# Performance work log

Hardware: AMD Instinct MI355X
Metric: run time of the kernel (lower is better)

Reference implementation:

```python
import jax, jax.numpy as jnp
import numpy as np

HID, NH, HD, KTS = 512, 8, 64, 4
BATCH, SEQ = 2, 1024
CLIP, AMIN, AMAX = 2.0, 1e-4, 0.9995
ROPE_BASE = 10000.0


def _rmsnorm(x, w, eps=1e-5):
    rms = jnp.sqrt(jnp.mean(x * x, axis=-1, keepdims=True) + eps)
    return x / rms * w


def _rope(q, k, base=ROPE_BASE):
    # q,k: [B,T,H,D], D even -> rotate-half formulation (split halves, not interleaved)
    T, D = q.shape[1], q.shape[-1]
    half = D // 2
    pos = jnp.arange(T, dtype=q.dtype)
    inv_freq = 1.0 / (base ** (jnp.arange(half, dtype=q.dtype) / half))
    ang = pos[:, None] * inv_freq[None, :]            # [T, half]
    cos = jnp.cos(ang)[None, :, None, :]
    sin = jnp.sin(ang)[None, :, None, :]
    def rot(x):
        x1, x2 = x[..., :half], x[..., half:]
        return jnp.concatenate([x1 * cos - x2 * sin, x1 * sin + x2 * cos], axis=-1)
    return rot(q), rot(k)


def setup_inputs() -> dict:
    key = jax.random.key(0)
    ks = jax.random.split(key, 10)
    def xavier(k, shape):
        lim = float(np.sqrt(6.0 / (shape[0] + shape[1])))
        return jax.random.uniform(k, shape, jnp.float32, -lim, lim)
    x = jax.random.normal(ks[0], (BATCH, SEQ, HID), jnp.float32)
    mask = jnp.ones((BATCH, SEQ), jnp.int32)
    qW = xavier(ks[1], (HID, HID))
    kW = xavier(ks[2], (HID, HID))
    vW = xavier(ks[3], (HID, HID))
    oW = xavier(ks[4], (HID, HID))
    ob = jnp.zeros((HID,), jnp.float32)
    # alpha bias from geometric half-lives [32,128,512,2048]
    half_lives = np.array([32.0 * (4.0 ** i) for i in range(KTS)], dtype=np.float64)
    alphas = np.clip(np.exp(-np.log(2.0) / half_lives), AMIN, AMAX)
    alphas = np.tile(alphas, NH)
    ab = jnp.asarray(np.log(alphas / (1.0 - alphas)), jnp.float32)
    aW = 0.01 * jax.random.normal(ks[5], (NH * KTS, HID), jnp.float32)
    mW = 0.01 * jax.random.normal(ks[6], (NH * KTS, HID), jnp.float32)
    mb = jnp.zeros((NH * KTS,), jnp.float32)
    in_w = jnp.ones((HID,), jnp.float32)
    kn_w = jnp.ones((HD,), jnp.float32)
    vn_w = jnp.ones((HD,), jnp.float32)
    ln_w = jnp.ones((HID,), jnp.float32)
    ln_b = jnp.zeros((HID,), jnp.float32)
    return dict(x=x, in_w=in_w, qW=qW, kW=kW, vW=vW, aW=aW, ab=ab, mW=mW, mb=mb,
                oW=oW, ob=ob, kn_w=kn_w, vn_w=vn_w, ln_w=ln_w, ln_b=ln_b, mask=mask)


def reference(x, in_w, qW, kW, vW, aW, ab, mW, mb, oW, ob, kn_w, vn_w, ln_w, ln_b, mask):
    B, T, _ = x.shape
    xn = _rmsnorm(x, in_w)
    q = (xn @ qW.T).reshape(B, T, NH, HD)
    k = (xn @ kW.T).reshape(B, T, NH, HD)
    v = (xn @ vW.T).reshape(B, T, NH, HD)
    q, k = _rope(q, k)
    k = _rmsnorm(k, kn_w)
    v = _rmsnorm(v, vn_w)
    alpha = jnp.clip(jax.nn.sigmoid(xn @ aW.T + ab), AMIN, AMAX).reshape(B, T, NH, KTS)
    mix = jax.nn.softmax((xn @ mW.T + mb).reshape(B, T, NH, KTS), axis=-1)
    m = mask.astype(jnp.float32)
    c = float(np.sqrt(HD)) * CLIP

    def step(h, inp):
        # h: [B,H,K,D,D] fp32 state; delta-rule write + multi-timescale decay + norm clip
        q_t, k_t, v_t, a_t, mx_t, m_t = inp
        outer = (k_t * m_t[:, None, None])[:, :, None, :, None] * v_t[:, :, None, None, :]
        h = h * a_t[..., None, None] + outer
        norm = jnp.sqrt(jnp.sum(h * h, axis=(-2, -1), keepdims=True))
        h = h * jnp.minimum(c / (norm + 1e-6), 1.0)
        y = jnp.einsum('bhd,bhkde->bhke', q_t, h)
        return h, jnp.einsum('bhk,bhkd->bhd', mx_t, y)

    h0 = jnp.zeros((B, NH, KTS, HD, HD), jnp.float32)
    tm = lambda a: jnp.moveaxis(a, 1, 0)  # time-major
    xs = (tm(q), tm(k), tm(v), tm(alpha), tm(mix), m.T)
    _, ys = jax.lax.scan(jax.checkpoint(step), h0, xs)  # ys: [T,B,H,D]
    y = jnp.moveaxis(ys, 0, 1).reshape(B, T, HID)
    out = y @ oW.T + ob  # dropout p=0 (eval)
    r = x + out
    mu = jnp.mean(r, axis=-1, keepdims=True)
    var = jnp.mean((r - mu) ** 2, axis=-1, keepdims=True)
    return (r - mu) / jnp.sqrt(var + 1e-5) * ln_w + ln_b
```

## Files before the change

### kernel.cpp

```cpp
#include <hip/hip_runtime.h>
#include <math.h>

#define SEQT 1024
#define NTOK 2048
#define HIDN 512
#define NHD 8
#define HDIM 64
#define KTSN 4

__device__ __forceinline__ float wred(float v) {
#pragma unroll
  for (int off = 32; off; off >>= 1) v += __shfl_xor(v, off, 64);
  return v;
}

template <int CTRL>
__device__ __forceinline__ float rra(float v) {
  return v + __int_as_float(__builtin_amdgcn_update_dpp(
                 0, __float_as_int(v), CTRL, 0xf, 0xf, true));
}
__device__ __forceinline__ float rlane(float v, int l) {
  return __int_as_float(__builtin_amdgcn_readlane(__float_as_int(v), l));
}
__device__ __forceinline__ float wsum64_fast(float v) {
  v = rra<0x121>(v);
  v = rra<0x122>(v);
  v = rra<0x124>(v);
  v = rra<0x128>(v);
  return (rlane(v, 0) + rlane(v, 16)) + (rlane(v, 32) + rlane(v, 48));
}

__global__ __launch_bounds__(256) void k_rmsnorm_in(
    const float* __restrict__ x, const float* __restrict__ w, float* __restrict__ xn) {
  int m = blockIdx.x;
  int tid = threadIdx.x;
  const float* row = x + (size_t)m * HIDN;
  float2 v = *(const float2*)(row + tid * 2);
  float ss = wred(v.x * v.x + v.y * v.y);
  __shared__ float red[4];
  int lane = tid & 63, wv = tid >> 6;
  if (lane == 0) red[wv] = ss;
  __syncthreads();
  float tot = red[0] + red[1] + red[2] + red[3];
  float inv = rsqrtf(tot * (1.0f / HIDN) + 1e-5f);
  float2 wv2 = *(const float2*)(w + tid * 2);
  float2 o;
  o.x = v.x * inv * wv2.x;
  o.y = v.y * inv * wv2.y;
  *(float2*)(xn + (size_t)m * HIDN + tid * 2) = o;
}

__global__ __launch_bounds__(256) void k_gemm_qkv(
    const float* __restrict__ A, const float* __restrict__ Bq,
    const float* __restrict__ Bk, const float* __restrict__ Bv,
    float* __restrict__ Cq, float* __restrict__ Ck, float* __restrict__ Cv) {
  __shared__ __align__(16) float As[32][68];
  __shared__ __align__(16) float Bs0[32][68];
  __shared__ __align__(16) float Bs1[32][68];
  __shared__ __align__(16) float Bs2[32][68];
  int tid = threadIdx.x;
  int m0 = blockIdx.x * 64, n0 = blockIdx.y * 64;
  int tm = tid >> 4, tn = tid & 15;
  float aq[4][4] = {}, ak[4][4] = {}, av4[4][4] = {};
  int rr = tid >> 2, cc = (tid & 3) * 8;
  for (int k0 = 0; k0 < HIDN; k0 += 32) {
    const float* s0 = A + (size_t)(m0 + rr) * HIDN + k0 + cc;
    float4 a0 = *(const float4*)s0;
    float4 a1 = *(const float4*)(s0 + 4);
    As[cc + 0][rr] = a0.x; As[cc + 1][rr] = a0.y; As[cc + 2][rr] = a0.z; As[cc + 3][rr] = a0.w;
    As[cc + 4][rr] = a1.x; As[cc + 5][rr] = a1.y; As[cc + 6][rr] = a1.z; As[cc + 7][rr] = a1.w;
    size_t boff = (size_t)(n0 + rr) * HIDN + k0 + cc;
    float4 b0 = *(const float4*)(Bq + boff);
    float4 b1 = *(const float4*)(Bq + boff + 4);
    Bs0[cc + 0][rr] = b0.x; Bs0[cc + 1][rr] = b0.y; Bs0[cc + 2][rr] = b0.z; Bs0[cc + 3][rr] = b0.w;
    Bs0[cc + 4][rr] = b1.x; Bs0[cc + 5][rr] = b1.y; Bs0[cc + 6][rr] = b1.z; Bs0[cc + 7][rr] = b1.w;
    b0 = *(const float4*)(Bk + boff);
    b1 = *(const float4*)(Bk + boff + 4);
    Bs1[cc + 0][rr] = b0.x; Bs1[cc + 1][rr] = b0.y; Bs1[cc + 2][rr] = b0.z; Bs1[cc + 3][rr] = b0.w;
    Bs1[cc + 4][rr] = b1.x; Bs1[cc + 5][rr] = b1.y; Bs1[cc + 6][rr] = b1.z; Bs1[cc + 7][rr] = b1.w;
    b0 = *(const float4*)(Bv + boff);
    b1 = *(const float4*)(Bv + boff + 4);
    Bs2[cc + 0][rr] = b0.x; Bs2[cc + 1][rr] = b0.y; Bs2[cc + 2][rr] = b0.z; Bs2[cc + 3][rr] = b0.w;
    Bs2[cc + 4][rr] = b1.x; Bs2[cc + 5][rr] = b1.y; Bs2[cc + 6][rr] = b1.z; Bs2[cc + 7][rr] = b1.w;
    __syncthreads();
#pragma unroll
    for (int kk = 0; kk < 32; ++kk) {
      float4 a4 = *(const float4*)&As[kk][tm * 4];
      float4 q4 = *(const float4*)&Bs0[kk][tn * 4];
      float4 k4 = *(const float4*)&Bs1[kk][tn * 4];
      float4 v4 = *(const float4*)&Bs2[kk][tn * 4];
      float aa[4] = {a4.x, a4.y, a4.z, a4.w};
      float qq[4] = {q4.x, q4.y, q4.z, q4.w};
      float kk_[4] = {k4.x, k4.y, k4.z, k4.w};
      float vv[4] = {v4.x, v4.y, v4.z, v4.w};
#pragma unroll
      for (int i = 0; i < 4; ++i)
#pragma unroll
        for (int j = 0; j < 4; ++j) {
          aq[i][j] = fmaf(aa[i], qq[j], aq[i][j]);
          ak[i][j] = fmaf(aa[i], kk_[j], ak[i][j]);
          av4[i][j] = fmaf(aa[i], vv[j], av4[i][j]);
        }
    }
    __syncthreads();
  }
#pragma unroll
  for (int i = 0; i < 4; ++i) {
    size_t mr = (size_t)(m0 + tm * 4 + i) * HIDN;
#pragma unroll
    for (int j = 0; j < 4; ++j) {
      int nc = n0 + tn * 4 + j;
      Cq[mr + nc] = aq[i][j];
      Ck[mr + nc] = ak[i][j];
      Cv[mr + nc] = av4[i][j];
    }
  }
}

__global__ __launch_bounds__(256) void k_gemm_am(
    const float* __restrict__ A, const float* __restrict__ Ba,
    const float* __restrict__ Bm, float* __restrict__ Ca, float* __restrict__ Cm) {
  __shared__ __align__(16) float As[32][68];
  __shared__ __align__(16) float Bs[32][68];
  int tid = threadIdx.x;
  int m0 = blockIdx.x * 64;
  int tm = tid >> 4, tn = tid & 15;
  float acc[4][4] = {};
  int rr = tid >> 2, cc = (tid & 3) * 8;
  for (int k0 = 0; k0 < HIDN; k0 += 32) {
    const float* s0 = A + (size_t)(m0 + rr) * HIDN + k0 + cc;
    float4 a0 = *(const float4*)s0;
    float4 a1 = *(const float4*)(s0 + 4);
    As[cc + 0][rr] = a0.x; As[cc + 1][rr] = a0.y; As[cc + 2][rr] = a0.z; As[cc + 3][rr] = a0.w;
    As[cc + 4][rr] = a1.x; As[cc + 5][rr] = a1.y; As[cc + 6][rr] = a1.z; As[cc + 7][rr] = a1.w;
    const float* s1 = ((rr < 32) ? (Ba + (size_t)rr * HIDN) : (Bm + (size_t)(rr - 32) * HIDN)) + k0 + cc;
    float4 b0 = *(const float4*)s1;
    float4 b1 = *(const float4*)(s1 + 4);
    Bs[cc + 0][rr] = b0.x; Bs[cc + 1][rr] = b0.y; Bs[cc + 2][rr] = b0.z; Bs[cc + 3][rr] = b0.w;
    Bs[cc + 4][rr] = b1.x; Bs[cc + 5][rr] = b1.y; Bs[cc + 6][rr] = b1.z; Bs[cc + 7][rr] = b1.w;
    __syncthreads();
#pragma unroll
    for (int kk = 0; kk < 32; ++kk) {
      float4 a4 = *(const float4*)&As[kk][tm * 4];
      float4 b4 = *(const float4*)&Bs[kk][tn * 4];
      float aa[4] = {a4.x, a4.y, a4.z, a4.w};
      float bb[4] = {b4.x, b4.y, b4.z, b4.w};
#pragma unroll
      for (int i = 0; i < 4; ++i)
#pragma unroll
        for (int j = 0; j < 4; ++j) acc[i][j] = fmaf(aa[i], bb[j], acc[i][j]);
    }
    __syncthreads();
  }
#pragma unroll
  for (int i = 0; i < 4; ++i) {
    int mr = m0 + tm * 4 + i;
#pragma unroll
    for (int j = 0; j < 4; ++j) {
      int nc = tn * 4 + j;
      if (nc < 32)
        Ca[(size_t)mr * 32 + nc] = acc[i][j];
      else
        Cm[(size_t)mr * 32 + nc - 32] = acc[i][j];
    }
  }
}

__global__ __launch_bounds__(256) void k_rope_table(float2* __restrict__ tab) {
  int idx = blockIdx.x * 256 + threadIdx.x;
  int t = idx >> 5, j = idx & 31;
  float invf = (float)exp2(-(double)j * (13.287712379549449 / 32.0));
  float ang = (float)t * invf;
  double s, c;
  sincos((double)ang, &s, &c);
  tab[idx] = make_float2((float)c, (float)s);
}

__global__ __launch_bounds__(256) void k_postproc(
    const float* __restrict__ q_in, const float* __restrict__ k_in, const float* __restrict__ v_in,
    const float* __restrict__ a_pre, const float* __restrict__ m_pre,
    const float* __restrict__ ab, const float* __restrict__ mb,
    const float* __restrict__ kn_w, const float* __restrict__ vn_w,
    const float2* __restrict__ tab,
    float* __restrict__ qh, float* __restrict__ kh, float* __restrict__ vh,
    float* __restrict__ av, float* __restrict__ mv,
    float* __restrict__ qkd, float* __restrict__ kvq) {
  int wid = blockIdx.x * 4 + (threadIdx.x >> 6);
  int lane = threadIdx.x & 63;
  int b = wid >> 13;
  int rem = wid & 8191;
  int t = rem >> 3;
  int h = rem & 7;
  size_t src = (size_t)(b * SEQT + t) * HIDN + h * HDIM + lane;
  float qv = q_in[src], kv = k_in[src], vv = v_in[src];
  float2 cs = tab[t * 32 + (lane & 31)];
  float qpart = __shfl_xor(qv, 32, 64);
  float kpart = __shfl_xor(kv, 32, 64);
  float qr = (lane < 32) ? (qv * cs.x - qpart * cs.y) : (qpart * cs.y + qv * cs.x);
  float kr = (lane < 32) ? (kv * cs.x - kpart * cs.y) : (kpart * cs.y + kv * cs.x);
  float kss = wred(kr * kr);
  float kn = kr * rsqrtf(kss * (1.0f / HDIM) + 1e-5f) * kn_w[lane];
  float vss = wred(vv * vv);
  float vn = vv * rsqrtf(vss * (1.0f / HDIM) + 1e-5f) * vn_w[lane];
  size_t dst = ((size_t)(b * NHD + h) * SEQT + t) * HDIM + lane;
  qh[dst] = qr;
  kh[dst] = kn;
  vh[dst] = vn;
  float knss = wred(kn * kn);
  float vnss = wred(vn * vn);
  float qkdot = wred(qr * kn);
  if (lane == 0) {
    size_t sdst = (size_t)(b * NHD + h) * SEQT + t;
    qkd[sdst] = qkdot;
    kvq[sdst] = knss * vnss;
  }
  if (lane < 4) {
    int col = h * 4 + lane;
    float pa = a_pre[(size_t)(b * SEQT + t) * 32 + col] + ab[col];
    float al = 1.0f / (1.0f + expf(-pa));
    al = fminf(fmaxf(al, 1e-4f), 0.9995f);
    float pm = m_pre[(size_t)(b * SEQT + t) * 32 + col] + mb[col];
    float mx = pm;
    mx = fmaxf(mx, __shfl_xor(mx, 1, 64));
    mx = fmaxf(mx, __shfl_xor(mx, 2, 64));
    float e = expf(pm - mx);
    float sum = e;
    sum += __shfl_xor(sum, 1, 64);
    sum += __shfl_xor(sum, 2, 64);
    size_t adst = ((size_t)(b * NHD + h) * KTSN + lane) * SEQT + t;
    av[adst] = al;
    mv[adst] = e / sum;
  }
}

__global__ __launch_bounds__(256) void k_cross(
    const float* __restrict__ qh, const float* __restrict__ kh, const float* __restrict__ vh,
    float* __restrict__ kkx, float* __restrict__ vvx, float* __restrict__ qxx) {
  int wid = blockIdx.x * 4 + (threadIdx.x >> 6);
  int lane = threadIdx.x & 63;
  int bh = wid >> 10;
  int t = wid & 1023;
  size_t sidx = (size_t)bh * SEQT + t;
  if (t == 0) {
    if (lane == 0) { kkx[sidx] = 0.f; vvx[sidx] = 0.f; qxx[sidx] = 0.f; }
    return;
  }
  size_t base = (size_t)bh * SEQT * HDIM;
  float kc = kh[base + (size_t)t * HDIM + lane];
  float kp = kh[base + (size_t)(t - 1) * HDIM + lane];
  float vc = vh[base + (size_t)t * HDIM + lane];
  float vpv = vh[base + (size_t)(t - 1) * HDIM + lane];
  float qc = qh[base + (size_t)t * HDIM + lane];
  float s1 = wred(kc * kp);
  float s2 = wred(vc * vpv);
  float s3 = wred(qc * kp);
  if (lane == 0) { kkx[sidx] = s1; vvx[sidx] = s2; qxx[sidx] = s3; }
}

#define G16P(X) \
  X(0, 0) X(1, 1) X(2, 2) X(3, 3) X(4, 0) X(5, 1) X(6, 2) X(7, 3) \
  X(8, 0) X(9, 1) X(10, 2) X(11, 3) X(12, 0) X(13, 1) X(14, 2) X(15, 3)

#define DECLH(g, a) float h##g = 0.f;
#define HUP0(g, a) h##g = fmaf(h##g, ag0, rlane(kqj0, (g)) * vm0);
#define HUP1(g, a) h##g = fmaf(h##g, ag1, rlane(kqj1, (g)) * vm1);
#define MV4(g, a)                                   \
  {                                                 \
    float k2_ = rlane(kqj2, (g));                   \
    float q2_ = rlane(kqj2, 16 + (g));              \
    float k3_ = rlane(kqj3, (g));                   \
    float q3_ = rlane(kqj3, 16 + (g));              \
    zk2##a = fmaf(k2_, h##g, zk2##a);               \
    zk3##a = fmaf(k3_, h##g, zk3##a);               \
    pv2##a = fmaf(q2_, h##g, pv2##a);               \
    pv3##a = fmaf(q3_, h##g, pv3##a);               \
  }

__global__ __launch_bounds__(256, 1) void k_scan(
    const float* __restrict__ qh, const float* __restrict__ kh, const float* __restrict__ vh,
    const float* __restrict__ av, const float* __restrict__ mv, const int* __restrict__ mask,
    const float* __restrict__ qkd, const float* __restrict__ kvq,
    const float* __restrict__ kkx, const float* __restrict__ vvx, const float* __restrict__ qxx,
    float* __restrict__ y0p, float* __restrict__ y1p, float* __restrict__ y2p,
    float* __restrict__ y3p) {
  int c = blockIdx.x;
  int kt = c & 3;
  int bh = c >> 2;
  int b = bh >> 3;
  int h = bh & 7;
  int tid = threadIdx.x;
  int w = tid >> 6;
  int lane = tid & 63;
  int dbase = w * 16;

  const float* kp = kh + (size_t)bh * SEQT * HDIM;
  const float* qp = qh + (size_t)bh * SEQT * HDIM;
  const float* vp = vh + (size_t)bh * SEQT * HDIM;
  const float* ap = av + (size_t)c * SEQT;
  const float* mp = mv + (size_t)c * SEQT;
  const float* qkp = qkd + (size_t)bh * SEQT;
  const float* kvp = kvq + (size_t)bh * SEQT;
  const float* kkp = kkx + (size_t)bh * SEQT;
  const float* vvp = vvx + (size_t)bh * SEQT;
  const float* qxp = qxx + (size_t)bh * SEQT;
  const int* mk = mask + (size_t)b * SEQT;
  float* ysel = (kt == 0) ? y0p : (kt == 1) ? y1p : (kt == 2) ? y2p : y3p;
  float* ypo = ysel + (size_t)(b * SEQT) * HIDN + h * HDIM + lane;

  __shared__ __align__(16) float2 Zb[2][4];
  __shared__ __align__(16) float Pb[2][2][4][64];
  __shared__ int cnt;

  G16P(DECLH)
  float gprev = 1.0f;
  float usq = 0.0f;

  int off = lane & 15;
  const float* kqbase = ((lane >> 4) & 1) ? qp : kp;
  int kqidx = dbase + off;

  float kqj0 = kqbase[kqidx];
  float kqj1 = kqbase[(size_t)1 * HDIM + kqidx];
  float kqj2 = kqbase[(size_t)2 * HDIM + kqidx];
  float kqj3 = kqbase[(size_t)3 * HDIM + kqidx];
  float kqj4 = kqbase[(size_t)4 * HDIM + kqidx];
  float kqj5 = kqbase[(size_t)5 * HDIM + kqidx];
  float vj0 = vp[lane], vj1 = vp[HDIM + lane], vj2 = vp[2 * HDIM + lane];
  float vj3 = vp[3 * HDIM + lane], vj4 = vp[4 * HDIM + lane], vj5 = vp[5 * HDIM + lane];
  float a0 = ap[0], a1 = ap[1], a2 = ap[2], a3 = ap[3], a4 = ap[4], a5 = ap[5];
  float mx0 = mp[0], mx1 = mp[1], mx2 = mp[2], mx3 = mp[3], mx4 = mp[4], mx5 = mp[5];
  float m0 = (float)mk[0], m1 = (float)mk[1], m2 = (float)mk[2];
  float m3 = (float)mk[3], m4 = (float)mk[4], m5 = (float)mk[5];
  float qk0 = qkp[0], qk1 = qkp[1], qk2 = qkp[2], qk3 = qkp[3], qk4 = qkp[4], qk5 = qkp[5];
  float kv0 = kvp[0], kv1 = kvp[1], kv2 = kvp[2], kv3 = kvp[3], kv4 = kvp[4], kv5 = kvp[5];
  float kko0 = kkp[1], kko1 = kkp[3], kko2 = kkp[5];
  float vvo0 = vvp[1], vvo1 = vvp[3], vvo2 = vvp[5];
  float qxo0 = qxp[1], qxo1 = qxp[3], qxo2 = qxp[5];

  if (tid == 0) cnt = 0;
  if (lane == 0) Zb[0][w] = make_float2(0.f, 0.f);
  Pb[0][0][w][lane] = 0.f;
  Pb[0][1][w][lane] = 0.f;
  __syncthreads();

  for (int s = 0; s < SEQT; s += 2) {
    int r = s >> 1;
    int P = r & 1;
    int t6 = s + 6, t7 = s + 7;
    if (t6 > SEQT - 1) t6 = SEQT - 1;
    if (t7 > SEQT - 1) t7 = SEQT - 1;
    float kqN6 = kqbase[(size_t)t6 * HDIM + kqidx];
    float kqN7 = kqbase[(size_t)t7 * HDIM + kqidx];
    float vN6 = vp[(size_t)t6 * HDIM + lane];
    float vN7 = vp[(size_t)t7 * HDIM + lane];
    float aN6 = ap[t6], aN7 = ap[t7];
    float mxN6 = mp[t6], mxN7 = mp[t7];
    float mN6 = (float)mk[t6], mN7 = (float)mk[t7];
    float qkN6 = qkp[t6], qkN7 = qkp[t7];
    float kvN6 = kvp[t6], kvN7 = kvp[t7];
    float kkN = kkp[t7], vvN = vvp[t7], qxN = qxp[t7];

    float2 zb0 = Zb[P][0], zb1 = Zb[P][1], zb2 = Zb[P][2], zb3 = Zb[P][3];
    float zs = (zb0.x + zb1.x) + (zb2.x + zb3.x);
    float w1 = (zb0.y + zb1.y) + (zb2.y + zb3.y);

    float ag0 = a0 * gprev;
    float vm0 = m0 * vj0;
    G16P(HUP0)
    float usq0 = fmaf(ag0 * ag0, usq, fmaf(2.0f * ag0 * m0, zs, (m0 * m0) * kv0));
    usq0 = fmaxf(usq0, 0.0f);
    float g0 = fminf(16.0f * rsqrtf(usq0), 1.0f);

    float z1 = fmaf(ag0, w1, (m0 * kko0) * vvo0);
    float ag1 = a1 * g0;
    float vm1 = m1 * vj1;
    G16P(HUP1)
    float usq1 = fmaf(ag1 * ag1, usq0, fmaf(2.0f * ag1 * m1, z1, (m1 * m1) * kv1));
    usq1 = fmaxf(usq1, 0.0f);
    float g1 = fminf(16.0f * rsqrtf(usq1), 1.0f);

    float zk20 = 0.f, zk21 = 0.f, zk22 = 0.f, zk23 = 0.f;
    float zk30 = 0.f, zk31 = 0.f, zk32 = 0.f, zk33 = 0.f;
    float pv20 = 0.f, pv21 = 0.f, pv22 = 0.f, pv23 = 0.f;
    float pv30 = 0.f, pv31 = 0.f, pv32 = 0.f, pv33 = 0.f;
    G16P(MV4)
    float zk2s = (zk20 + zk21) + (zk22 + zk23);
    float zk3s = (zk30 + zk31) + (zk32 + zk33);
    float Z0n = wsum64_fast(zk2s * vj2);
    float Z1n = wsum64_fast(zk3s * vj3);
    float P0n = (pv20 + pv21) + (pv22 + pv23);
    float P1n = (pv30 + pv31) + (pv32 + pv33);

    if (w == 0) {
      float pe = (Pb[P][0][0][lane] + Pb[P][0][1][lane]) +
                 (Pb[P][0][2][lane] + Pb[P][0][3][lane]);
      ypo[(size_t)s * HIDN] = (g0 * mx0) * fmaf(ag0, pe, (m0 * qk0) * vj0);
    } else if (w == 1) {
      float pe = (Pb[P][1][0][lane] + Pb[P][1][1][lane]) +
                 (Pb[P][1][2][lane] + Pb[P][1][3][lane]);
      float p1 = fmaf(ag0, pe, (m0 * qxo0) * vj0);
      ypo[(size_t)(s + 1) * HIDN] = (g1 * mx1) * fmaf(ag1, p1, (m1 * qk1) * vj1);
    }

    if (lane == 0) Zb[P ^ 1][w] = make_float2(Z0n, Z1n);
    Pb[P ^ 1][0][w][lane] = P0n;
    Pb[P ^ 1][1][w][lane] = P1n;
    asm volatile("s_waitcnt lgkmcnt(0)" ::: "memory");
    if (lane == 0) atomicAdd(&cnt, 1);
    {
      int target = 4 * (r + 1);
      while (*(volatile int*)&cnt < target) {
      }
    }
    asm volatile("" ::: "memory");

    gprev = g1;
    usq = usq1;
    kqj0 = kqj2; kqj1 = kqj3; kqj2 = kqj4; kqj3 = kqj5; kqj4 = kqN6; kqj5 = kqN7;
    vj0 = vj2; vj1 = vj3; vj2 = vj4; vj3 = vj5; vj4 = vN6; vj5 = vN7;
    a0 = a2; a1 = a3; a2 = a4; a3 = a5; a4 = aN6; a5 = aN7;
    mx0 = mx2; mx1 = mx3; mx2 = mx4; mx3 = mx5; mx4 = mxN6; mx5 = mxN7;
    m0 = m2; m1 = m3; m2 = m4; m3 = m5; m4 = mN6; m5 = mN7;
    qk0 = qk2; qk1 = qk3; qk2 = qk4; qk3 = qk5; qk4 = qkN6; qk5 = qkN7;
    kv0 = kv2; kv1 = kv3; kv2 = kv4; kv3 = kv5; kv4 = kvN6; kv5 = kvN7;
    kko0 = kko1; kko1 = kko2; kko2 = kkN;
    vvo0 = vvo1; vvo1 = vvo2; vvo2 = vvN;
    qxo0 = qxo1; qxo1 = qxo2; qxo2 = qxN;
  }
}

__global__ __launch_bounds__(256) void k_gemm_out(
    const float* __restrict__ y0, const float* __restrict__ y1,
    const float* __restrict__ y2, const float* __restrict__ y3,
    const float* __restrict__ oW, const float* __restrict__ ob,
    const float* __restrict__ x, float* __restrict__ r) {
  __shared__ __align__(16) float As[32][68];
  __shared__ __align__(16) float Bs[32][68];
  int tid = threadIdx.x;
  int m0 = blockIdx.x * 64, n0 = blockIdx.y * 64;
  int tm = tid >> 4, tn = tid & 15;
  float acc[4][4] = {};
  int rr = tid >> 2, cc = (tid & 3) * 8;
  for (int k0 = 0; k0 < HIDN; k0 += 32) {
    size_t aoff = (size_t)(m0 + rr) * HIDN + k0 + cc;
#pragma unroll
    for (int half = 0; half < 2; ++half) {
      size_t sh = aoff + half * 4;
      float4 p0 = *(const float4*)(y0 + sh);
      float4 p1 = *(const float4*)(y1 + sh);
      float4 p2 = *(const float4*)(y2 + sh);
      float4 p3 = *(const float4*)(y3 + sh);
      int cbase = cc + half * 4;
      As[cbase + 0][rr] = p0.x + p1.x + p2.x + p3.x;
      As[cbase + 1][rr] = p0.y + p1.y + p2.y + p3.y;
      As[cbase + 2][rr] = p0.z + p1.z + p2.z + p3.z;
      As[cbase + 3][rr] = p0.w + p1.w + p2.w + p3.w;
    }
    const float* s1 = oW + (size_t)(n0 + rr) * HIDN + k0 + cc;
    float4 b0 = *(const float4*)s1;
    float4 b1 = *(const float4*)(s1 + 4);
    Bs[cc + 0][rr] = b0.x; Bs[cc + 1][rr] = b0.y; Bs[cc + 2][rr] = b0.z; Bs[cc + 3][rr] = b0.w;
    Bs[cc + 4][rr] = b1.x; Bs[cc + 5][rr] = b1.y; Bs[cc + 6][rr] = b1.z; Bs[cc + 7][rr] = b1.w;
    __syncthreads();
#pragma unroll
    for (int kk = 0; kk < 32; ++kk) {
      float4 a4 = *(const float4*)&As[kk][tm * 4];
      float4 b4 = *(const float4*)&Bs[kk][tn * 4];
      float aa[4] = {a4.x, a4.y, a4.z, a4.w};
      float bb[4] = {b4.x, b4.y, b4.z, b4.w};
#pragma unroll
      for (int i = 0; i < 4; ++i)
#pragma unroll
        for (int j = 0; j < 4; ++j) acc[i][j] += aa[i] * bb[j];
    }
    __syncthreads();
  }
#pragma unroll
  for (int i = 0; i < 4; ++i) {
    int mr = m0 + tm * 4 + i;
#pragma unroll
    for (int j = 0; j < 4; ++j) {
      int nc = n0 + tn * 4 + j;
      r[(size_t)mr * HIDN + nc] = x[(size_t)mr * HIDN + nc] + acc[i][j] + ob[nc];
    }
  }
}

__global__ __launch_bounds__(256) void k_layernorm(
    const float* __restrict__ r, const float* __restrict__ w, const float* __restrict__ bb,
    float* __restrict__ out) {
  int m = blockIdx.x;
  int tid = threadIdx.x;
  const float* row = r + (size_t)m * HIDN;
  float2 v = *(const float2*)(row + tid * 2);
  float s = wred(v.x + v.y);
  float ss = wred(v.x * v.x + v.y * v.y);
  __shared__ float r1[4], r2[4];
  int lane = tid & 63, wv = tid >> 6;
  if (lane == 0) {
    r1[wv] = s;
    r2[wv] = ss;
  }
  __syncthreads();
  float S = r1[0] + r1[1] + r1[2] + r1[3];
  float SS = r2[0] + r2[1] + r2[2] + r2[3];
  float mu = S * (1.0f / HIDN);
  float var = SS * (1.0f / HIDN) - mu * mu;
  float inv = rsqrtf(var + 1e-5f);
  float2 w2 = *(const float2*)(w + tid * 2);
  float2 b2 = *(const float2*)(bb + tid * 2);
  float2 o;
  o.x = (v.x - mu) * inv * w2.x + b2.x;
  o.y = (v.y - mu) * inv * w2.y + b2.y;
  *(float2*)(out + (size_t)m * HIDN + tid * 2) = o;
}

extern "C" void kernel_launch(void* const* d_in, const int* in_sizes, int n_in,
                              void* d_out, int out_size, void* d_ws, size_t ws_size,
                              hipStream_t stream) {
  const float* x = (const float*)d_in[0];
  const float* in_w = (const float*)d_in[1];
  const float* qW = (const float*)d_in[2];
  const float* kW = (const float*)d_in[3];
  const float* vW = (const float*)d_in[4];
  const float* aW = (const float*)d_in[5];
  const float* ab = (const float*)d_in[6];
  const float* mW = (const float*)d_in[7];
  const float* mb = (const float*)d_in[8];
  const float* oW = (const float*)d_in[9];
  const float* ob = (const float*)d_in[10];
  const float* kn_w = (const float*)d_in[11];
  const float* vn_w = (const float*)d_in[12];
  const float* ln_w = (const float*)d_in[13];
  const float* ln_b = (const float*)d_in[14];
  const int* mask = (const int*)d_in[15];

  float* ws = (float*)d_ws;
  float* xn = ws + 0;
  float* qb = ws + 1048576;
  float* kb = ws + 2097152;
  float* vb = ws + 3145728;
  float* apre = ws + 4194304;
  float* mpre = ws + 4259840;
  float2* tab = (float2*)(ws + 4325376);
  float* qh = ws + 4390912;
  float* kh = ws + 5439488;
  float* vh = ws + 6488064;
  float* avv = ws + 7536640;
  float* mvv = ws + 7602176;
  float* y3 = ws + 7667712;
  float* y0 = qb;
  float* y1 = kb;
  float* y2 = vb;
  float* rr = xn;
  float* qkd = ws + 0;
  float* kvq = ws + 16384;
  float* kkx = ws + 32768;
  float* vvx = ws + 49152;
  float* qxx = ws + 65536;

  k_rope_table<<<128, 256, 0, stream>>>(tab);
  k_rmsnorm_in<<<NTOK, 256, 0, stream>>>(x, in_w, xn);
  dim3 gBig(32, 8);
  k_gemm_qkv<<<gBig, 256, 0, stream>>>(xn, qW, kW, vW, qb, kb, vb);
  k_gemm_am<<<32, 256, 0, stream>>>(xn, aW, mW, apre, mpre);
  k_postproc<<<4096, 256, 0, stream>>>(qb, kb, vb, apre, mpre, ab, mb, kn_w, vn_w, tab,
                                       qh, kh, vh, avv, mvv, qkd, kvq);
  k_cross<<<4096, 256, 0, stream>>>(qh, kh, vh, kkx, vvx, qxx);
  k_scan<<<64, 256, 0, stream>>>(qh, kh, vh, avv, mvv, mask, qkd, kvq, kkx, vvx, qxx,
                                 y0, y1, y2, y3);
  k_gemm_out<<<gBig, 256, 0, stream>>>(y0, y1, y2, y3, oW, ob, x, rr);
  k_layernorm<<<NTOK, 256, 0, stream>>>(rr, ln_w, ln_b, (float*)d_out);
  (void)in_sizes; (void)n_in; (void)out_size; (void)ws_size;
}
```

Baseline: 702.0 us.

## Split scan state rows across eight waves instead of four

```diff
diff --git a/kernel.cpp b/kernel.cpp
--- a/kernel.cpp
+++ b/kernel.cpp
@@ -257,9 +257,8 @@
   if (lane == 0) { kkx[sidx] = s1; vvx[sidx] = s2; qxx[sidx] = s3; }
 }
 
-#define G16P(X) \
-  X(0, 0) X(1, 1) X(2, 2) X(3, 3) X(4, 0) X(5, 1) X(6, 2) X(7, 3) \
-  X(8, 0) X(9, 1) X(10, 2) X(11, 3) X(12, 0) X(13, 1) X(14, 2) X(15, 3)
+#define G8P(X) \
+  X(0, 0) X(1, 1) X(2, 2) X(3, 3) X(4, 0) X(5, 1) X(6, 2) X(7, 3)
 
 #define DECLH(g, a) float h##g = 0.f;
 #define HUP0(g, a) h##g = fmaf(h##g, ag0, rlane(kqj0, (g)) * vm0);
@@ -267,16 +266,16 @@
 #define MV4(g, a)                                   \
   {                                                 \
     float k2_ = rlane(kqj2, (g));                   \
-    float q2_ = rlane(kqj2, 16 + (g));              \
+    float q2_ = rlane(kqj2, 8 + (g));               \
     float k3_ = rlane(kqj3, (g));                   \
-    float q3_ = rlane(kqj3, 16 + (g));              \
+    float q3_ = rlane(kqj3, 8 + (g));               \
     zk2##a = fmaf(k2_, h##g, zk2##a);               \
     zk3##a = fmaf(k3_, h##g, zk3##a);               \
     pv2##a = fmaf(q2_, h##g, pv2##a);               \
     pv3##a = fmaf(q3_, h##g, pv3##a);               \
   }
 
-__global__ __launch_bounds__(256, 1) void k_scan(
+__global__ __launch_bounds__(512, 1) void k_scan(
     const float* __restrict__ qh, const float* __restrict__ kh, const float* __restrict__ vh,
     const float* __restrict__ av, const float* __restrict__ mv, const int* __restrict__ mask,
     const float* __restrict__ qkd, const float* __restrict__ kvq,
@@ -291,7 +290,7 @@
   int tid = threadIdx.x;
   int w = tid >> 6;
   int lane = tid & 63;
-  int dbase = w * 16;
+  int dbase = w * 8;
 
   const float* kp = kh + (size_t)bh * SEQT * HDIM;
   const float* qp = qh + (size_t)bh * SEQT * HDIM;
@@ -307,16 +306,17 @@
   float* ysel = (kt == 0) ? y0p : (kt == 1) ? y1p : (kt == 2) ? y2p : y3p;
   float* ypo = ysel + (size_t)(b * SEQT) * HIDN + h * HDIM + lane;
 
-  __shared__ __align__(16) float2 Zb[2][4];
-  __shared__ __align__(16) float Pb[2][2][4][64];
+  __shared__ __align__(16) float Z0b[2][8];
+  __shared__ __align__(16) float Z1b[2][8];
+  __shared__ __align__(16) float Pb[2][2][8][64];
   __shared__ int cnt;
 
-  G16P(DECLH)
+  G8P(DECLH)
   float gprev = 1.0f;
   float usq = 0.0f;
 
-  int off = lane & 15;
-  const float* kqbase = ((lane >> 4) & 1) ? qp : kp;
+  int off = lane & 7;
+  const float* kqbase = ((lane >> 3) & 1) ? qp : kp;
   int kqidx = dbase + off;
 
   float kqj0 = kqbase[kqidx];
@@ -338,7 +338,7 @@
   float qxo0 = qxp[1], qxo1 = qxp[3], qxo2 = qxp[5];
 
   if (tid == 0) cnt = 0;
-  if (lane == 0) Zb[0][w] = make_float2(0.f, 0.f);
+  if (lane == 0) { Z0b[0][w] = 0.f; Z1b[0][w] = 0.f; }
   Pb[0][0][w][lane] = 0.f;
   Pb[0][1][w][lane] = 0.f;
   __syncthreads();
@@ -360,13 +360,16 @@
     float kvN6 = kvp[t6], kvN7 = kvp[t7];
     float kkN = kkp[t7], vvN = vvp[t7], qxN = qxp[t7];
 
-    float2 zb0 = Zb[P][0], zb1 = Zb[P][1], zb2 = Zb[P][2], zb3 = Zb[P][3];
-    float zs = (zb0.x + zb1.x) + (zb2.x + zb3.x);
-    float w1 = (zb0.y + zb1.y) + (zb2.y + zb3.y);
+    float4 za = *(const float4*)&Z0b[P][0];
+    float4 zb = *(const float4*)&Z0b[P][4];
+    float zs = ((za.x + za.y) + (za.z + za.w)) + ((zb.x + zb.y) + (zb.z + zb.w));
+    float4 wa = *(const float4*)&Z1b[P][0];
+    float4 wb = *(const float4*)&Z1b[P][4];
+    float w1 = ((wa.x + wa.y) + (wa.z + wa.w)) + ((wb.x + wb.y) + (wb.z + wb.w));
 
     float ag0 = a0 * gprev;
     float vm0 = m0 * vj0;
-    G16P(HUP0)
+    G8P(HUP0)
     float usq0 = fmaf(ag0 * ag0, usq, fmaf(2.0f * ag0 * m0, zs, (m0 * m0) * kv0));
     usq0 = fmaxf(usq0, 0.0f);
     float g0 = fminf(16.0f * rsqrtf(usq0), 1.0f);
@@ -374,7 +377,7 @@
     float z1 = fmaf(ag0, w1, (m0 * kko0) * vvo0);
     float ag1 = a1 * g0;
     float vm1 = m1 * vj1;
-    G16P(HUP1)
+    G8P(HUP1)
     float usq1 = fmaf(ag1 * ag1, usq0, fmaf(2.0f * ag1 * m1, z1, (m1 * m1) * kv1));
     usq1 = fmaxf(usq1, 0.0f);
     float g1 = fminf(16.0f * rsqrtf(usq1), 1.0f);
@@ -383,7 +386,7 @@
     float zk30 = 0.f, zk31 = 0.f, zk32 = 0.f, zk33 = 0.f;
     float pv20 = 0.f, pv21 = 0.f, pv22 = 0.f, pv23 = 0.f;
     float pv30 = 0.f, pv31 = 0.f, pv32 = 0.f, pv33 = 0.f;
-    G16P(MV4)
+    G8P(MV4)
     float zk2s = (zk20 + zk21) + (zk22 + zk23);
     float zk3s = (zk30 + zk31) + (zk32 + zk33);
     float Z0n = wsum64_fast(zk2s * vj2);
@@ -392,23 +395,27 @@
     float P1n = (pv30 + pv31) + (pv32 + pv33);
 
     if (w == 0) {
-      float pe = (Pb[P][0][0][lane] + Pb[P][0][1][lane]) +
-                 (Pb[P][0][2][lane] + Pb[P][0][3][lane]);
+      float pe = ((Pb[P][0][0][lane] + Pb[P][0][1][lane]) +
+                  (Pb[P][0][2][lane] + Pb[P][0][3][lane])) +
+                 ((Pb[P][0][4][lane] + Pb[P][0][5][lane]) +
+                  (Pb[P][0][6][lane] + Pb[P][0][7][lane]));
       ypo[(size_t)s * HIDN] = (g0 * mx0) * fmaf(ag0, pe, (m0 * qk0) * vj0);
     } else if (w == 1) {
-      float pe = (Pb[P][1][0][lane] + Pb[P][1][1][lane]) +
-                 (Pb[P][1][2][lane] + Pb[P][1][3][lane]);
+      float pe = ((Pb[P][1][0][lane] + Pb[P][1][1][lane]) +
+                  (Pb[P][1][2][lane] + Pb[P][1][3][lane])) +
+                 ((Pb[P][1][4][lane] + Pb[P][1][5][lane]) +
+                  (Pb[P][1][6][lane] + Pb[P][1][7][lane]));
       float p1 = fmaf(ag0, pe, (m0 * qxo0) * vj0);
       ypo[(size_t)(s + 1) * HIDN] = (g1 * mx1) * fmaf(ag1, p1, (m1 * qk1) * vj1);
     }
 
-    if (lane == 0) Zb[P ^ 1][w] = make_float2(Z0n, Z1n);
+    if (lane == 0) { Z0b[P ^ 1][w] = Z0n; Z1b[P ^ 1][w] = Z1n; }
     Pb[P ^ 1][0][w][lane] = P0n;
     Pb[P ^ 1][1][w][lane] = P1n;
     asm volatile("s_waitcnt lgkmcnt(0)" ::: "memory");
     if (lane == 0) atomicAdd(&cnt, 1);
     {
-      int target = 4 * (r + 1);
+      int target = 8 * (r + 1);
       while (*(volatile int*)&cnt < target) {
       }
     }
@@ -567,7 +574,7 @@
   k_postproc<<<4096, 256, 0, stream>>>(qb, kb, vb, apre, mpre, ab, mb, kn_w, vn_w, tab,
                                        qh, kh, vh, avv, mvv, qkd, kvq);
   k_cross<<<4096, 256, 0, stream>>>(qh, kh, vh, kkx, vvx, qxx);
-  k_scan<<<64, 256, 0, stream>>>(qh, kh, vh, avv, mvv, mask, qkd, kvq, kkx, vvx, qxx,
+  k_scan<<<64, 512, 0, stream>>>(qh, kh, vh, avv, mvv, mask, qkd, kvq, kkx, vvx, qxx,
                                  y0, y1, y2, y3);
   k_gemm_out<<<gBig, 256, 0, stream>>>(y0, y1, y2, y3, oW, ob, x, rr);
   k_layernorm<<<NTOK, 256, 0, stream>>>(rr, ln_w, ln_b, (float*)d_out);
```

Measured after the change: 753.7 us. 1.07x slower.

## Interleave two timescale chains per scan block to hide barrier latency

Applied to the files above, without the earlier changes.

```diff
diff --git a/kernel.cpp b/kernel.cpp
--- a/kernel.cpp
+++ b/kernel.cpp
@@ -261,19 +261,32 @@
   X(0, 0) X(1, 1) X(2, 2) X(3, 3) X(4, 0) X(5, 1) X(6, 2) X(7, 3) \
   X(8, 0) X(9, 1) X(10, 2) X(11, 3) X(12, 0) X(13, 1) X(14, 2) X(15, 3)
 
-#define DECLH(g, a) float h##g = 0.f;
-#define HUP0(g, a) h##g = fmaf(h##g, ag0, rlane(kqj0, (g)) * vm0);
-#define HUP1(g, a) h##g = fmaf(h##g, ag1, rlane(kqj1, (g)) * vm1);
-#define MV4(g, a)                                   \
+#define DECLH(g, a) float hA##g = 0.f, hB##g = 0.f;
+#define HUP0A(g, a) hA##g = fmaf(hA##g, ag0, rlane(kqj0, (g)) * vm0);
+#define HUP1A(g, a) hA##g = fmaf(hA##g, ag1, rlane(kqj1, (g)) * vm1);
+#define HUP0B(g, a) hB##g = fmaf(hB##g, ag0, rlane(kqj0, (g)) * vm0);
+#define HUP1B(g, a) hB##g = fmaf(hB##g, ag1, rlane(kqj1, (g)) * vm1);
+#define MV4A(g, a)                                  \
   {                                                 \
     float k2_ = rlane(kqj2, (g));                   \
     float q2_ = rlane(kqj2, 16 + (g));              \
     float k3_ = rlane(kqj3, (g));                   \
     float q3_ = rlane(kqj3, 16 + (g));              \
-    zk2##a = fmaf(k2_, h##g, zk2##a);               \
-    zk3##a = fmaf(k3_, h##g, zk3##a);               \
-    pv2##a = fmaf(q2_, h##g, pv2##a);               \
-    pv3##a = fmaf(q3_, h##g, pv3##a);               \
+    zk2##a = fmaf(k2_, hA##g, zk2##a);              \
+    zk3##a = fmaf(k3_, hA##g, zk3##a);              \
+    pv2##a = fmaf(q2_, hA##g, pv2##a);              \
+    pv3##a = fmaf(q3_, hA##g, pv3##a);              \
+  }
+#define MV4B(g, a)                                  \
+  {                                                 \
+    float k2_ = rlane(kqj2, (g));                   \
+    float q2_ = rlane(kqj2, 16 + (g));              \
+    float k3_ = rlane(kqj3, (g));                   \
+    float q3_ = rlane(kqj3, 16 + (g));              \
+    zk2##a = fmaf(k2_, hB##g, zk2##a);              \
+    zk3##a = fmaf(k3_, hB##g, zk3##a);              \
+    pv2##a = fmaf(q2_, hB##g, pv2##a);              \
+    pv3##a = fmaf(q3_, hB##g, pv3##a);              \
   }
 
 __global__ __launch_bounds__(256, 1) void k_scan(
@@ -283,9 +296,9 @@
     const float* __restrict__ kkx, const float* __restrict__ vvx, const float* __restrict__ qxx,
     float* __restrict__ y0p, float* __restrict__ y1p, float* __restrict__ y2p,
     float* __restrict__ y3p) {
-  int c = blockIdx.x;
-  int kt = c & 3;
-  int bh = c >> 2;
+  int bhp = blockIdx.x;
+  int bh = bhp >> 1;
+  int pair = bhp & 1;
   int b = bh >> 3;
   int h = bh & 7;
   int tid = threadIdx.x;
@@ -296,24 +309,30 @@
   const float* kp = kh + (size_t)bh * SEQT * HDIM;
   const float* qp = qh + (size_t)bh * SEQT * HDIM;
   const float* vp = vh + (size_t)bh * SEQT * HDIM;
-  const float* ap = av + (size_t)c * SEQT;
-  const float* mp = mv + (size_t)c * SEQT;
+  const float* apA = av + (size_t)(bh * 4 + 2 * pair + 0) * SEQT;
+  const float* apB = av + (size_t)(bh * 4 + 2 * pair + 1) * SEQT;
+  const float* mpA = mv + (size_t)(bh * 4 + 2 * pair + 0) * SEQT;
+  const float* mpB = mv + (size_t)(bh * 4 + 2 * pair + 1) * SEQT;
   const float* qkp = qkd + (size_t)bh * SEQT;
   const float* kvp = kvq + (size_t)bh * SEQT;
   const float* kkp = kkx + (size_t)bh * SEQT;
   const float* vvp = vvx + (size_t)bh * SEQT;
   const float* qxp = qxx + (size_t)bh * SEQT;
   const int* mk = mask + (size_t)b * SEQT;
-  float* ysel = (kt == 0) ? y0p : (kt == 1) ? y1p : (kt == 2) ? y2p : y3p;
-  float* ypo = ysel + (size_t)(b * SEQT) * HIDN + h * HDIM + lane;
-
-  __shared__ __align__(16) float2 Zb[2][4];
-  __shared__ __align__(16) float Pb[2][2][4][64];
-  __shared__ int cnt;
+  float* yselA = (pair == 0) ? y0p : y2p;
+  float* yselB = (pair == 0) ? y1p : y3p;
+  float* ypoA = yselA + (size_t)(b * SEQT) * HIDN + h * HDIM + lane;
+  float* ypoB = yselB + (size_t)(b * SEQT) * HIDN + h * HDIM + lane;
+
+  __shared__ __align__(16) float2 ZA[2][4];
+  __shared__ __align__(16) float2 ZB[2][4];
+  __shared__ __align__(16) float PbA[2][2][4][64];
+  __shared__ __align__(16) float PbB[2][2][4][64];
+  __shared__ int cntA, cntB;
 
   G16P(DECLH)
-  float gprev = 1.0f;
-  float usq = 0.0f;
+  float gprevA = 1.0f, usqA = 0.0f;
+  float gprevB = 1.0f, usqB = 0.0f;
 
   int off = lane & 15;
   const float* kqbase = ((lane >> 4) & 1) ? qp : kp;
@@ -327,8 +346,6 @@
   float kqj5 = kqbase[(size_t)5 * HDIM + kqidx];
   float vj0 = vp[lane], vj1 = vp[HDIM + lane], vj2 = vp[2 * HDIM + lane];
   float vj3 = vp[3 * HDIM + lane], vj4 = vp[4 * HDIM + lane], vj5 = vp[5 * HDIM + lane];
-  float a0 = ap[0], a1 = ap[1], a2 = ap[2], a3 = ap[3], a4 = ap[4], a5 = ap[5];
-  float mx0 = mp[0], mx1 = mp[1], mx2 = mp[2], mx3 = mp[3], mx4 = mp[4], mx5 = mp[5];
   float m0 = (float)mk[0], m1 = (float)mk[1], m2 = (float)mk[2];
   float m3 = (float)mk[3], m4 = (float)mk[4], m5 = (float)mk[5];
   float qk0 = qkp[0], qk1 = qkp[1], qk2 = qkp[2], qk3 = qkp[3], qk4 = qkp[4], qk5 = qkp[5];
@@ -336,11 +353,15 @@
   float kko0 = kkp[1], kko1 = kkp[3], kko2 = kkp[5];
   float vvo0 = vvp[1], vvo1 = vvp[3], vvo2 = vvp[5];
   float qxo0 = qxp[1], qxo1 = qxp[3], qxo2 = qxp[5];
-
-  if (tid == 0) cnt = 0;
-  if (lane == 0) Zb[0][w] = make_float2(0.f, 0.f);
-  Pb[0][0][w][lane] = 0.f;
-  Pb[0][1][w][lane] = 0.f;
+  float aA0 = apA[0], aA1 = apA[1], aA2 = apA[2], aA3 = apA[3], aA4 = apA[4], aA5 = apA[5];
+  float aB0 = apB[0], aB1 = apB[1], aB2 = apB[2], aB3 = apB[3], aB4 = apB[4], aB5 = apB[5];
+  float mxA0 = mpA[0], mxA1 = mpA[1], mxA2 = mpA[2], mxA3 = mpA[3], mxA4 = mpA[4], mxA5 = mpA[5];
+  float mxB0 = mpB[0], mxB1 = mpB[1], mxB2 = mpB[2], mxB3 = mpB[3], mxB4 = mpB[4], mxB5 = mpB[5];
+
+  if (tid == 0) { cntA = 0; cntB = 0; }
+  if (lane == 0) { ZA[0][w] = make_float2(0.f, 0.f); ZB[0][w] = make_float2(0.f, 0.f); }
+  PbA[0][0][w][lane] = 0.f; PbA[0][1][w][lane] = 0.f;
+  PbB[0][0][w][lane] = 0.f; PbB[0][1][w][lane] = 0.f;
   __syncthreads();
 
   for (int s = 0; s < SEQT; s += 2) {
@@ -353,79 +374,136 @@
     float kqN7 = kqbase[(size_t)t7 * HDIM + kqidx];
     float vN6 = vp[(size_t)t6 * HDIM + lane];
     float vN7 = vp[(size_t)t7 * HDIM + lane];
-    float aN6 = ap[t6], aN7 = ap[t7];
-    float mxN6 = mp[t6], mxN7 = mp[t7];
     float mN6 = (float)mk[t6], mN7 = (float)mk[t7];
     float qkN6 = qkp[t6], qkN7 = qkp[t7];
     float kvN6 = kvp[t6], kvN7 = kvp[t7];
     float kkN = kkp[t7], vvN = vvp[t7], qxN = qxp[t7];
-
-    float2 zb0 = Zb[P][0], zb1 = Zb[P][1], zb2 = Zb[P][2], zb3 = Zb[P][3];
-    float zs = (zb0.x + zb1.x) + (zb2.x + zb3.x);
-    float w1 = (zb0.y + zb1.y) + (zb2.y + zb3.y);
-
-    float ag0 = a0 * gprev;
+    float aAN6 = apA[t6], aAN7 = apA[t7], aBN6 = apB[t6], aBN7 = apB[t7];
+    float mxAN6 = mpA[t6], mxAN7 = mpA[t7], mxBN6 = mpB[t6], mxBN7 = mpB[t7];
+
     float vm0 = m0 * vj0;
-    G16P(HUP0)
-    float usq0 = fmaf(ag0 * ag0, usq, fmaf(2.0f * ag0 * m0, zs, (m0 * m0) * kv0));
-    usq0 = fmaxf(usq0, 0.0f);
-    float g0 = fminf(16.0f * rsqrtf(usq0), 1.0f);
-
-    float z1 = fmaf(ag0, w1, (m0 * kko0) * vvo0);
-    float ag1 = a1 * g0;
     float vm1 = m1 * vj1;
-    G16P(HUP1)
-    float usq1 = fmaf(ag1 * ag1, usq0, fmaf(2.0f * ag1 * m1, z1, (m1 * m1) * kv1));
-    usq1 = fmaxf(usq1, 0.0f);
-    float g1 = fminf(16.0f * rsqrtf(usq1), 1.0f);
-
-    float zk20 = 0.f, zk21 = 0.f, zk22 = 0.f, zk23 = 0.f;
-    float zk30 = 0.f, zk31 = 0.f, zk32 = 0.f, zk33 = 0.f;
-    float pv20 = 0.f, pv21 = 0.f, pv22 = 0.f, pv23 = 0.f;
-    float pv30 = 0.f, pv31 = 0.f, pv32 = 0.f, pv33 = 0.f;
-    G16P(MV4)
-    float zk2s = (zk20 + zk21) + (zk22 + zk23);
-    float zk3s = (zk30 + zk31) + (zk32 + zk33);
-    float Z0n = wsum64_fast(zk2s * vj2);
-    float Z1n = wsum64_fast(zk3s * vj3);
-    float P0n = (pv20 + pv21) + (pv22 + pv23);
-    float P1n = (pv30 + pv31) + (pv32 + pv33);
-
-    if (w == 0) {
-      float pe = (Pb[P][0][0][lane] + Pb[P][0][1][lane]) +
-                 (Pb[P][0][2][lane] + Pb[P][0][3][lane]);
-      ypo[(size_t)s * HIDN] = (g0 * mx0) * fmaf(ag0, pe, (m0 * qk0) * vj0);
-    } else if (w == 1) {
-      float pe = (Pb[P][1][0][lane] + Pb[P][1][1][lane]) +
-                 (Pb[P][1][2][lane] + Pb[P][1][3][lane]);
-      float p1 = fmaf(ag0, pe, (m0 * qxo0) * vj0);
-      ypo[(size_t)(s + 1) * HIDN] = (g1 * mx1) * fmaf(ag1, p1, (m1 * qk1) * vj1);
-    }
-
-    if (lane == 0) Zb[P ^ 1][w] = make_float2(Z0n, Z1n);
-    Pb[P ^ 1][0][w][lane] = P0n;
-    Pb[P ^ 1][1][w][lane] = P1n;
-    asm volatile("s_waitcnt lgkmcnt(0)" ::: "memory");
-    if (lane == 0) atomicAdd(&cnt, 1);
+
     {
-      int target = 4 * (r + 1);
-      while (*(volatile int*)&cnt < target) {
+      int target = 4 * r;
+      while (*(volatile int*)&cntA < target) {
       }
     }
     asm volatile("" ::: "memory");
-
-    gprev = g1;
-    usq = usq1;
+    {
+      float2 zb0 = ZA[P][0], zb1 = ZA[P][1], zb2 = ZA[P][2], zb3 = ZA[P][3];
+      float zs = (zb0.x + zb1.x) + (zb2.x + zb3.x);
+      float w1 = (zb0.y + zb1.y) + (zb2.y + zb3.y);
+
+      float ag0 = aA0 * gprevA;
+      G16P(HUP0A)
+      float usq0 = fmaf(ag0 * ag0, usqA, fmaf(2.0f * ag0 * m0, zs, (m0 * m0) * kv0));
+      usq0 = fmaxf(usq0, 0.0f);
+      float g0 = fminf(16.0f * rsqrtf(usq0), 1.0f);
+
+      float z1 = fmaf(ag0, w1, (m0 * kko0) * vvo0);
+      float ag1 = aA1 * g0;
+      G16P(HUP1A)
+      float usq1 = fmaf(ag1 * ag1, usq0, fmaf(2.0f * ag1 * m1, z1, (m1 * m1) * kv1));
+      usq1 = fmaxf(usq1, 0.0f);
+      float g1 = fminf(16.0f * rsqrtf(usq1), 1.0f);
+
+      float zk20 = 0.f, zk21 = 0.f, zk22 = 0.f, zk23 = 0.f;
+      float zk30 = 0.f, zk31 = 0.f, zk32 = 0.f, zk33 = 0.f;
+      float pv20 = 0.f, pv21 = 0.f, pv22 = 0.f, pv23 = 0.f;
+      float pv30 = 0.f, pv31 = 0.f, pv32 = 0.f, pv33 = 0.f;
+      G16P(MV4A)
+      float Z0n = wsum64_fast(((zk20 + zk21) + (zk22 + zk23)) * vj2);
+      float Z1n = wsum64_fast(((zk30 + zk31) + (zk32 + zk33)) * vj3);
+      float P0n = (pv20 + pv21) + (pv22 + pv23);
+      float P1n = (pv30 + pv31) + (pv32 + pv33);
+
+      if (w == 0) {
+        float pe = (PbA[P][0][0][lane] + PbA[P][0][1][lane]) +
+                   (PbA[P][0][2][lane] + PbA[P][0][3][lane]);
+        ypoA[(size_t)s * HIDN] = (g0 * mxA0) * fmaf(ag0, pe, (m0 * qk0) * vj0);
+      } else if (w == 1) {
+        float pe = (PbA[P][1][0][lane] + PbA[P][1][1][lane]) +
+                   (PbA[P][1][2][lane] + PbA[P][1][3][lane]);
+        float p1 = fmaf(ag0, pe, (m0 * qxo0) * vj0);
+        ypoA[(size_t)(s + 1) * HIDN] = (g1 * mxA1) * fmaf(ag1, p1, (m1 * qk1) * vj1);
+      }
+
+      if (lane == 0) ZA[P ^ 1][w] = make_float2(Z0n, Z1n);
+      PbA[P ^ 1][0][w][lane] = P0n;
+      PbA[P ^ 1][1][w][lane] = P1n;
+      asm volatile("s_waitcnt lgkmcnt(0)" ::: "memory");
+      if (lane == 0) atomicAdd(&cntA, 1);
+      gprevA = g1;
+      usqA = usq1;
+    }
+
+    {
+      int target = 4 * r;
+      while (*(volatile int*)&cntB < target) {
+      }
+    }
+    asm volatile("" ::: "memory");
+    {
+      float2 zb0 = ZB[P][0], zb1 = ZB[P][1], zb2 = ZB[P][2], zb3 = ZB[P][3];
+      float zs = (zb0.x + zb1.x) + (zb2.x + zb3.x);
+      float w1 = (zb0.y + zb1.y) + (zb2.y + zb3.y);
+
+      float ag0 = aB0 * gprevB;
+      G16P(HUP0B)
+      float usq0 = fmaf(ag0 * ag0, usqB, fmaf(2.0f * ag0 * m0, zs, (m0 * m0) * kv0));
+      usq0 = fmaxf(usq0, 0.0f);
+      float g0 = fminf(16.0f * rsqrtf(usq0), 1.0f);
+
+      float z1 = fmaf(ag0, w1, (m0 * kko0) * vvo0);
+      float ag1 = aB1 * g0;
+      G16P(HUP1B)
+      float usq1 = fmaf(ag1 * ag1, usq0, fmaf(2.0f * ag1 * m1, z1, (m1 * m1) * kv1));
+      usq1 = fmaxf(usq1, 0.0f);
+      float g1 = fminf(16.0f * rsqrtf(usq1), 1.0f);
+
+      float zk20 = 0.f, zk21 = 0.f, zk22 = 0.f, zk23 = 0.f;
+      float zk30 = 0.f, zk31 = 0.f, zk32 = 0.f, zk33 = 0.f;
+      float pv20 = 0.f, pv21 = 0.f, pv22 = 0.f, pv23 = 0.f;
+      float pv30 = 0.f, pv31 = 0.f, pv32 = 0.f, pv33 = 0.f;
+      G16P(MV4B)
+      float Z0n = wsum64_fast(((zk20 + zk21) + (zk22 + zk23)) * vj2);
+      float Z1n = wsum64_fast(((zk30 + zk31) + (zk32 + zk33)) * vj3);
+      float P0n = (pv20 + pv21) + (pv22 + pv23);
+      float P1n = (pv30 + pv31) + (pv32 + pv33);
+
+      if (w == 2) {
+        float pe = (PbB[P][0][0][lane] + PbB[P][0][1][lane]) +
+                   (PbB[P][0][2][lane] + PbB[P][0][3][lane]);
+        ypoB[(size_t)s * HIDN] = (g0 * mxB0) * fmaf(ag0, pe, (m0 * qk0) * vj0);
+      } else if (w == 3) {
+        float pe = (PbB[P][1][0][lane] + PbB[P][1][1][lane]) +
+                   (PbB[P][1][2][lane] + PbB[P][1][3][lane]);
+        float p1 = fmaf(ag0, pe, (m0 * qxo0) * vj0);
+        ypoB[(size_t)(s + 1) * HIDN] = (g1 * mxB1) * fmaf(ag1, p1, (m1 * qk1) * vj1);
+      }
+
+      if (lane == 0) ZB[P ^ 1][w] = make_float2(Z0n, Z1n);
+      PbB[P ^ 1][0][w][lane] = P0n;
+      PbB[P ^ 1][1][w][lane] = P1n;
+      asm volatile("s_waitcnt lgkmcnt(0)" ::: "memory");
+      if (lane == 0) atomicAdd(&cntB, 1);
+      gprevB = g1;
+      usqB = usq1;
+    }
+
     kqj0 = kqj2; kqj1 = kqj3; kqj2 = kqj4; kqj3 = kqj5; kqj4 = kqN6; kqj5 = kqN7;
     vj0 = vj2; vj1 = vj3; vj2 = vj4; vj3 = vj5; vj4 = vN6; vj5 = vN7;
-    a0 = a2; a1 = a3; a2 = a4; a3 = a5; a4 = aN6; a5 = aN7;
-    mx0 = mx2; mx1 = mx3; mx2 = mx4; mx3 = mx5; mx4 = mxN6; mx5 = mxN7;
     m0 = m2; m1 = m3; m2 = m4; m3 = m5; m4 = mN6; m5 = mN7;
     qk0 = qk2; qk1 = qk3; qk2 = qk4; qk3 = qk5; qk4 = qkN6; qk5 = qkN7;
     kv0 = kv2; kv1 = kv3; kv2 = kv4; kv3 = kv5; kv4 = kvN6; kv5 = kvN7;
     kko0 = kko1; kko1 = kko2; kko2 = kkN;
     vvo0 = vvo1; vvo1 = vvo2; vvo2 = vvN;
     qxo0 = qxo1; qxo1 = qxo2; qxo2 = qxN;
+    aA0 = aA2; aA1 = aA3; aA2 = aA4; aA3 = aA5; aA4 = aAN6; aA5 = aAN7;
+    aB0 = aB2; aB1 = aB3; aB2 = aB4; aB3 = aB5; aB4 = aBN6; aB5 = aBN7;
+    mxA0 = mxA2; mxA1 = mxA3; mxA2 = mxA4; mxA3 = mxA5; mxA4 = mxAN6; mxA5 = mxAN7;
+    mxB0 = mxB2; mxB1 = mxB3; mxB2 = mxB4; mxB3 = mxB5; mxB4 = mxBN6; mxB5 = mxBN7;
   }
 }
 
@@ -567,7 +645,7 @@
   k_postproc<<<4096, 256, 0, stream>>>(qb, kb, vb, apre, mpre, ab, mb, kn_w, vn_w, tab,
                                        qh, kh, vh, avv, mvv, qkd, kvq);
   k_cross<<<4096, 256, 0, stream>>>(qh, kh, vh, kkx, vvx, qxx);
-  k_scan<<<64, 256, 0, stream>>>(qh, kh, vh, avv, mvv, mask, qkd, kvq, kkx, vvx, qxx,
+  k_scan<<<32, 256, 0, stream>>>(qh, kh, vh, avv, mvv, mask, qkd, kvq, kkx, vvx, qxx,
                                  y0, y1, y2, y3);
   k_gemm_out<<<gBig, 256, 0, stream>>>(y0, y1, y2, y3, oW, ob, x, rr);
   k_layernorm<<<NTOK, 256, 0, stream>>>(rr, ln_w, ln_b, (float*)d_out);
```

Result: slower. 1.382 ms (+96.9%).
